# Kernel tuning notes

Measured on AMD Instinct MI355X. Metric: run time of the kernel, lower is better.

The kernel has to match this reference:

```python
import jax, jax.numpy as jnp
import numpy as np

B, S, ENC, DEC = 64, 4096, 512, 512


def setup_inputs() -> dict:
    key = jax.random.key(0)
    k1, k2, k3 = jax.random.split(key, 3)
    decoderFeature = jax.random.normal(k1, (B, 1, DEC), dtype=jnp.float32)
    encoderFeature = jax.random.normal(k2, (B, S, ENC), dtype=jnp.float32)
    # xavier_uniform for W: [enc, dec]
    limit = float(np.sqrt(6.0 / (ENC + DEC)))
    W = jax.random.uniform(k3, (ENC, DEC), dtype=jnp.float32, minval=-limit, maxval=limit)
    return {"decoderFeature": decoderFeature, "encoderFeature": encoderFeature, "W": W}


def reference(decoderFeature, encoderFeature, W):
    # F.linear(x, W) = x @ W.T : [B,1,dec] -> [B,1,enc]
    sub = jnp.einsum('bqd,ed->bqe', decoderFeature, W)
    # scores: [B,1,S]
    attn = jnp.einsum('bqe,bse->bqs', sub, encoderFeature)
    attn = jax.nn.softmax(attn, axis=2)
    # weighted sum: [B, enc]
    sumResult = jnp.einsum('bqs,bse->bqe', attn, encoderFeature).reshape(attn.shape[0], -1)
    return attn, sumResult
```

## Files before the change

kernel.cpp:

```cpp
#include <hip/hip_runtime.h>
#include <math.h>

#define BB   64
#define SS   4096
#define ENC  512
#define DEC  512
#define NSPLIT 16
#define CHUNK (SS / NSPLIT)

__global__ __launch_bounds__(256) void k_sub(const float* __restrict__ dec,
                                             const float* __restrict__ W,
                                             float* __restrict__ sub) {
    const int b    = blockIdx.y;
    const int lane = threadIdx.x & 63;
    const int wave = threadIdx.x >> 6;

    const float4* dv = (const float4*)(dec + (size_t)b * DEC);
    float4 q0 = dv[lane * 2 + 0];
    float4 q1 = dv[lane * 2 + 1];

    const int e0 = blockIdx.x * 128 + wave * 32;
    for (int i = 0; i < 32; ++i) {
        const int e = e0 + i;
        const float4* wv = (const float4*)(W + (size_t)e * DEC);
        float4 w0 = wv[lane * 2 + 0];
        float4 w1 = wv[lane * 2 + 1];
        float p = q0.x * w0.x + q0.y * w0.y + q0.z * w0.z + q0.w * w0.w
                + q1.x * w1.x + q1.y * w1.y + q1.z * w1.z + q1.w * w1.w;
        #pragma unroll
        for (int off = 32; off >= 1; off >>= 1) p += __shfl_xor(p, off, 64);
        if (lane == 0) sub[(size_t)b * ENC + e] = p;
    }
}

__global__ __launch_bounds__(256) void k_attn(const float* __restrict__ enc,
                                              const float* __restrict__ sub,
                                              float* __restrict__ attn_raw,
                                              float* __restrict__ chunk_m,
                                              float* __restrict__ chunk_l,
                                              float* __restrict__ chunk_acc) {
    const int b    = blockIdx.y;
    const int c    = blockIdx.x;
    const int lane = threadIdx.x & 63;
    const int wave = threadIdx.x >> 6;

    const float4* qv = (const float4*)(sub + (size_t)b * ENC);
    float4 q0 = qv[lane * 2 + 0];
    float4 q1 = qv[lane * 2 + 1];

    float m = -INFINITY, l = 0.f;
    float4 a0 = {0.f, 0.f, 0.f, 0.f};
    float4 a1 = {0.f, 0.f, 0.f, 0.f};

    const int sBase = c * CHUNK;
    #pragma unroll 2
    for (int i = wave; i < CHUNK; i += 4) {
        const int s = sBase + i;
        const float4* ev = (const float4*)(enc + ((size_t)b * SS + s) * ENC);
        float4 e0 = ev[lane * 2 + 0];
        float4 e1 = ev[lane * 2 + 1];

        float p = q0.x * e0.x + q0.y * e0.y + q0.z * e0.z + q0.w * e0.w
                + q1.x * e1.x + q1.y * e1.y + q1.z * e1.z + q1.w * e1.w;
        #pragma unroll
        for (int off = 32; off >= 1; off >>= 1) p += __shfl_xor(p, off, 64);

        if (lane == 0) attn_raw[(size_t)b * SS + s] = p;

        const float mn    = fmaxf(m, p);
        const float alpha = __expf(m - mn);
        const float w     = __expf(p - mn);
        l = l * alpha + w;
        a0.x = a0.x * alpha + w * e0.x;  a0.y = a0.y * alpha + w * e0.y;
        a0.z = a0.z * alpha + w * e0.z;  a0.w = a0.w * alpha + w * e0.w;
        a1.x = a1.x * alpha + w * e1.x;  a1.y = a1.y * alpha + w * e1.y;
        a1.z = a1.z * alpha + w * e1.z;  a1.w = a1.w * alpha + w * e1.w;
        m = mn;
    }

    __shared__ float sm[4];
    __shared__ float sl[4];
    __shared__ float sacc[4][ENC];

    if (lane == 0) sm[wave] = m;
    __syncthreads();
    const float M = fmaxf(fmaxf(sm[0], sm[1]), fmaxf(sm[2], sm[3]));
    const float f = __expf(m - M);
    if (lane == 0) sl[wave] = l * f;
    float* sa = &sacc[wave][lane * 8];
    sa[0] = a0.x * f; sa[1] = a0.y * f; sa[2] = a0.z * f; sa[3] = a0.w * f;
    sa[4] = a1.x * f; sa[5] = a1.y * f; sa[6] = a1.z * f; sa[7] = a1.w * f;
    __syncthreads();

    const size_t idx = (size_t)b * NSPLIT + c;
    if (threadIdx.x == 0) {
        chunk_m[idx] = M;
        chunk_l[idx] = sl[0] + sl[1] + sl[2] + sl[3];
    }
    for (int e = threadIdx.x; e < ENC; e += 256) {
        chunk_acc[idx * ENC + e] = sacc[0][e] + sacc[1][e] + sacc[2][e] + sacc[3][e];
    }
}

__global__ __launch_bounds__(256) void k_final(const float* __restrict__ chunk_m,
                                               const float* __restrict__ chunk_l,
                                               const float* __restrict__ chunk_acc,
                                               float* __restrict__ attn,
                                               float* __restrict__ sumResult) {
    const int b = blockIdx.x;

    float M = -INFINITY;
    #pragma unroll
    for (int c = 0; c < NSPLIT; ++c) M = fmaxf(M, chunk_m[(size_t)b * NSPLIT + c]);

    float f[NSPLIT];
    float L = 0.f;
    #pragma unroll
    for (int c = 0; c < NSPLIT; ++c) {
        f[c] = __expf(chunk_m[(size_t)b * NSPLIT + c] - M);
        L += chunk_l[(size_t)b * NSPLIT + c] * f[c];
    }
    const float invL = 1.f / L;

    for (int e = threadIdx.x; e < ENC; e += 256) {
        float s = 0.f;
        #pragma unroll
        for (int c = 0; c < NSPLIT; ++c)
            s += chunk_acc[((size_t)b * NSPLIT + c) * ENC + e] * f[c];
        sumResult[(size_t)b * ENC + e] = s * invL;
    }

    for (int s = threadIdx.x; s < SS; s += 256) {
        const size_t i = (size_t)b * SS + s;
        attn[i] = __expf(attn[i] - M) * invL;
    }
}

extern "C" void kernel_launch(void* const* d_in, const int* in_sizes, int n_in,
                              void* d_out, int out_size, void* d_ws, size_t ws_size,
                              hipStream_t stream) {
    const float* dec = (const float*)d_in[0];
    const float* enc = (const float*)d_in[1];
    const float* W   = (const float*)d_in[2];

    float* out       = (float*)d_out;
    float* attn      = out;
    float* sumResult = out + (size_t)BB * SS;

    float* ws        = (float*)d_ws;
    float* sub       = ws;
    float* chunk_m   = sub + (size_t)BB * ENC;
    float* chunk_l   = chunk_m + (size_t)BB * NSPLIT;
    float* chunk_acc = chunk_l + (size_t)BB * NSPLIT;

    k_sub  <<<dim3(4, BB),      256, 0, stream>>>(dec, W, sub);
    k_attn <<<dim3(NSPLIT, BB), 256, 0, stream>>>(enc, sub, attn, chunk_m, chunk_l, chunk_acc);
    k_final<<<BB,               256, 0, stream>>>(chunk_m, chunk_l, chunk_acc, attn, sumResult);
}
```

Before: 707.4 us.

## Double split count, coalesce float4 loads, dual softmax streams, parallelize finalize

Raises the sequence split from 16 to 32 so more blocks run concurrently. Changes the per-lane float4 access pattern to lane and lane+64, so consecutive lanes read consecutive 16-byte words. Each wave now keeps two independent online-softmax accumulators over interleaved rows, giving more loads in flight and breaking the dependency chain at the cost of extra registers. The final kernel becomes a 2D grid so attention normalization is spread across NSPLIT blocks per batch, which means each block recomputes the global max and sum.

```diff
diff --git a/kernel.cpp b/kernel.cpp
--- a/kernel.cpp
+++ b/kernel.cpp
@@ -5,7 +5,7 @@
 #define SS   4096
 #define ENC  512
 #define DEC  512
-#define NSPLIT 16
+#define NSPLIT 32
 #define CHUNK (SS / NSPLIT)
 
 __global__ __launch_bounds__(256) void k_sub(const float* __restrict__ dec,
@@ -16,15 +16,15 @@
     const int wave = threadIdx.x >> 6;
 
     const float4* dv = (const float4*)(dec + (size_t)b * DEC);
-    float4 q0 = dv[lane * 2 + 0];
-    float4 q1 = dv[lane * 2 + 1];
+    float4 q0 = dv[lane];
+    float4 q1 = dv[lane + 64];
 
     const int e0 = blockIdx.x * 128 + wave * 32;
     for (int i = 0; i < 32; ++i) {
         const int e = e0 + i;
         const float4* wv = (const float4*)(W + (size_t)e * DEC);
-        float4 w0 = wv[lane * 2 + 0];
-        float4 w1 = wv[lane * 2 + 1];
+        float4 w0 = wv[lane];
+        float4 w1 = wv[lane + 64];
         float p = q0.x * w0.x + q0.y * w0.y + q0.z * w0.z + q0.w * w0.w
                 + q1.x * w1.x + q1.y * w1.y + q1.z * w1.z + q1.w * w1.w;
         #pragma unroll
@@ -45,51 +45,88 @@
     const int wave = threadIdx.x >> 6;
 
     const float4* qv = (const float4*)(sub + (size_t)b * ENC);
-    float4 q0 = qv[lane * 2 + 0];
-    float4 q1 = qv[lane * 2 + 1];
-
-    float m = -INFINITY, l = 0.f;
-    float4 a0 = {0.f, 0.f, 0.f, 0.f};
-    float4 a1 = {0.f, 0.f, 0.f, 0.f};
-
-    const int sBase = c * CHUNK;
+    float4 q0 = qv[lane];
+    float4 q1 = qv[lane + 64];
+
+    float mA = -INFINITY, lA = 0.f, mB = -INFINITY, lB = 0.f;
+    float4 aA0 = {0,0,0,0}, aA1 = {0,0,0,0};
+    float4 aB0 = {0,0,0,0}, aB1 = {0,0,0,0};
+
+    const int sBase = c * CHUNK + wave;
     #pragma unroll 2
-    for (int i = wave; i < CHUNK; i += 4) {
-        const int s = sBase + i;
-        const float4* ev = (const float4*)(enc + ((size_t)b * SS + s) * ENC);
-        float4 e0 = ev[lane * 2 + 0];
-        float4 e1 = ev[lane * 2 + 1];
-
-        float p = q0.x * e0.x + q0.y * e0.y + q0.z * e0.z + q0.w * e0.w
-                + q1.x * e1.x + q1.y * e1.y + q1.z * e1.z + q1.w * e1.w;
+    for (int j = 0; j < CHUNK / 4; j += 2) {
+        const int sA = sBase + 4 * j;
+        const int sB = sA + 4;
+        const float4* evA = (const float4*)(enc + ((size_t)b * SS + sA) * ENC);
+        const float4* evB = (const float4*)(enc + ((size_t)b * SS + sB) * ENC);
+        float4 eA0 = evA[lane];
+        float4 eA1 = evA[lane + 64];
+        float4 eB0 = evB[lane];
+        float4 eB1 = evB[lane + 64];
+
+        float pA = q0.x * eA0.x + q0.y * eA0.y + q0.z * eA0.z + q0.w * eA0.w
+                 + q1.x * eA1.x + q1.y * eA1.y + q1.z * eA1.z + q1.w * eA1.w;
+        float pB = q0.x * eB0.x + q0.y * eB0.y + q0.z * eB0.z + q0.w * eB0.w
+                 + q1.x * eB1.x + q1.y * eB1.y + q1.z * eB1.z + q1.w * eB1.w;
         #pragma unroll
-        for (int off = 32; off >= 1; off >>= 1) p += __shfl_xor(p, off, 64);
-
-        if (lane == 0) attn_raw[(size_t)b * SS + s] = p;
-
-        const float mn    = fmaxf(m, p);
-        const float alpha = __expf(m - mn);
-        const float w     = __expf(p - mn);
-        l = l * alpha + w;
-        a0.x = a0.x * alpha + w * e0.x;  a0.y = a0.y * alpha + w * e0.y;
-        a0.z = a0.z * alpha + w * e0.z;  a0.w = a0.w * alpha + w * e0.w;
-        a1.x = a1.x * alpha + w * e1.x;  a1.y = a1.y * alpha + w * e1.y;
-        a1.z = a1.z * alpha + w * e1.z;  a1.w = a1.w * alpha + w * e1.w;
-        m = mn;
-    }
+        for (int off = 32; off >= 1; off >>= 1) {
+            pA += __shfl_xor(pA, off, 64);
+            pB += __shfl_xor(pB, off, 64);
+        }
+
+        if (lane == 0) {
+            attn_raw[(size_t)b * SS + sA] = pA;
+            attn_raw[(size_t)b * SS + sB] = pB;
+        }
+
+        {
+            const float mn = fmaxf(mA, pA);
+            const float al = __expf(mA - mn);
+            const float w  = __expf(pA - mn);
+            lA = lA * al + w;
+            aA0.x = aA0.x * al + w * eA0.x;  aA0.y = aA0.y * al + w * eA0.y;
+            aA0.z = aA0.z * al + w * eA0.z;  aA0.w = aA0.w * al + w * eA0.w;
+            aA1.x = aA1.x * al + w * eA1.x;  aA1.y = aA1.y * al + w * eA1.y;
+            aA1.z = aA1.z * al + w * eA1.z;  aA1.w = aA1.w * al + w * eA1.w;
+            mA = mn;
+        }
+        {
+            const float mn = fmaxf(mB, pB);
+            const float al = __expf(mB - mn);
+            const float w  = __expf(pB - mn);
+            lB = lB * al + w;
+            aB0.x = aB0.x * al + w * eB0.x;  aB0.y = aB0.y * al + w * eB0.y;
+            aB0.z = aB0.z * al + w * eB0.z;  aB0.w = aB0.w * al + w * eB0.w;
+            aB1.x = aB1.x * al + w * eB1.x;  aB1.y = aB1.y * al + w * eB1.y;
+            aB1.z = aB1.z * al + w * eB1.z;  aB1.w = aB1.w * al + w * eB1.w;
+            mB = mn;
+        }
+    }
+
+    const float mW = fmaxf(mA, mB);
+    const float fA = __expf(mA - mW);
+    const float fB = __expf(mB - mW);
+    const float lw = lA * fA + lB * fB;
+    float4 a0, a1;
+    a0.x = aA0.x * fA + aB0.x * fB;  a0.y = aA0.y * fA + aB0.y * fB;
+    a0.z = aA0.z * fA + aB0.z * fB;  a0.w = aA0.w * fA + aB0.w * fB;
+    a1.x = aA1.x * fA + aB1.x * fB;  a1.y = aA1.y * fA + aB1.y * fB;
+    a1.z = aA1.z * fA + aB1.z * fB;  a1.w = aA1.w * fA + aB1.w * fB;
 
     __shared__ float sm[4];
     __shared__ float sl[4];
     __shared__ float sacc[4][ENC];
 
-    if (lane == 0) sm[wave] = m;
+    if (lane == 0) sm[wave] = mW;
     __syncthreads();
     const float M = fmaxf(fmaxf(sm[0], sm[1]), fmaxf(sm[2], sm[3]));
-    const float f = __expf(m - M);
-    if (lane == 0) sl[wave] = l * f;
-    float* sa = &sacc[wave][lane * 8];
-    sa[0] = a0.x * f; sa[1] = a0.y * f; sa[2] = a0.z * f; sa[3] = a0.w * f;
-    sa[4] = a1.x * f; sa[5] = a1.y * f; sa[6] = a1.z * f; sa[7] = a1.w * f;
+    const float f = __expf(mW - M);
+    if (lane == 0) sl[wave] = lw * f;
+    float* sa = &sacc[wave][0];
+    sa[4 * lane + 0]       = a0.x * f;  sa[4 * lane + 1]       = a0.y * f;
+    sa[4 * lane + 2]       = a0.z * f;  sa[4 * lane + 3]       = a0.w * f;
+    sa[256 + 4 * lane + 0] = a1.x * f;  sa[256 + 4 * lane + 1] = a1.y * f;
+    sa[256 + 4 * lane + 2] = a1.z * f;  sa[256 + 4 * lane + 3] = a1.w * f;
     __syncthreads();
 
     const size_t idx = (size_t)b * NSPLIT + c;
@@ -108,29 +145,33 @@
                                                float* __restrict__ attn,
                                                float* __restrict__ sumResult) {
     const int b = blockIdx.x;
+    const int y = blockIdx.y;
 
     float M = -INFINITY;
     #pragma unroll
     for (int c = 0; c < NSPLIT; ++c) M = fmaxf(M, chunk_m[(size_t)b * NSPLIT + c]);
-
-    float f[NSPLIT];
     float L = 0.f;
     #pragma unroll
-    for (int c = 0; c < NSPLIT; ++c) {
-        f[c] = __expf(chunk_m[(size_t)b * NSPLIT + c] - M);
-        L += chunk_l[(size_t)b * NSPLIT + c] * f[c];
-    }
+    for (int c = 0; c < NSPLIT; ++c)
+        L += chunk_l[(size_t)b * NSPLIT + c] * __expf(chunk_m[(size_t)b * NSPLIT + c] - M);
     const float invL = 1.f / L;
 
-    for (int e = threadIdx.x; e < ENC; e += 256) {
-        float s = 0.f;
+    if (y == 0) {
+        float f[NSPLIT];
         #pragma unroll
         for (int c = 0; c < NSPLIT; ++c)
-            s += chunk_acc[((size_t)b * NSPLIT + c) * ENC + e] * f[c];
-        sumResult[(size_t)b * ENC + e] = s * invL;
-    }
-
-    for (int s = threadIdx.x; s < SS; s += 256) {
+            f[c] = __expf(chunk_m[(size_t)b * NSPLIT + c] - M);
+        for (int e = threadIdx.x; e < ENC; e += 256) {
+            float s = 0.f;
+            #pragma unroll
+            for (int c = 0; c < NSPLIT; ++c)
+                s += chunk_acc[((size_t)b * NSPLIT + c) * ENC + e] * f[c];
+            sumResult[(size_t)b * ENC + e] = s * invL;
+        }
+    }
+
+    const int s0 = y * (SS / NSPLIT);
+    for (int s = s0 + threadIdx.x; s < s0 + SS / NSPLIT; s += 256) {
         const size_t i = (size_t)b * SS + s;
         attn[i] = __expf(attn[i] - M) * invL;
     }
@@ -153,7 +194,7 @@
     float* chunk_l   = chunk_m + (size_t)BB * NSPLIT;
     float* chunk_acc = chunk_l + (size_t)BB * NSPLIT;
 
-    k_sub  <<<dim3(4, BB),      256, 0, stream>>>(dec, W, sub);
-    k_attn <<<dim3(NSPLIT, BB), 256, 0, stream>>>(enc, sub, attn, chunk_m, chunk_l, chunk_acc);
-    k_final<<<BB,               256, 0, stream>>>(chunk_m, chunk_l, chunk_acc, attn, sumResult);
-}
+    k_sub  <<<dim3(4, BB),       256, 0, stream>>>(dec, W, sub);
+    k_attn <<<dim3(NSPLIT, BB),  256, 0, stream>>>(enc, sub, attn, chunk_m, chunk_l, chunk_acc);
+    k_final<<<dim3(BB, NSPLIT),  256, 0, stream>>>(chunk_m, chunk_l, chunk_acc, attn, sumResult);
+}
```

Measured after the change: 703.5 us. No clear change (-0.6%).
